# Optimization experiments

Hardware: AMD Instinct MI355X
Metric: run time of the kernel (lower is better)

The kernel has to match this reference:

```python
import jax, jax.numpy as jnp
import numpy as np

N = 50000   # nodes
E = 800000  # edges
D = 96      # feature dim


def setup_inputs() -> dict:
    key = jax.random.key(0)
    k1, k2, k3, k4 = jax.random.split(key, 4)
    scale = 1.0 / np.sqrt(D)
    return {
        "x": jax.random.normal(k1, (N, D), dtype=jnp.float32),
        "edge_index": jax.random.randint(k2, (2, E), 0, N, dtype=jnp.int64),
        "W1": jax.random.normal(k3, (D, D), dtype=jnp.float32) * scale,
        "b1": jnp.zeros((D,), dtype=jnp.float32),
        "W2": jax.random.normal(k4, (D, D), dtype=jnp.float32) * scale,
        "b2": jnp.zeros((D,), dtype=jnp.float32),
    }


def _gcn_conv(x, src, dst, W, b, n_nodes):
    # PyG GCNConv: linear transform, add self-loops, symmetric normalization,
    # scatter-add aggregation from src (row) to dst (col), then bias.
    h = x @ W  # [N, D_out]
    loops = jnp.arange(n_nodes, dtype=src.dtype)
    s = jnp.concatenate([src, loops])  # [E+N]
    d = jnp.concatenate([dst, loops])  # [E+N]
    deg = jax.ops.segment_sum(jnp.ones_like(d, dtype=h.dtype), d, num_segments=n_nodes)
    dinv = jnp.where(deg > 0, jax.lax.rsqrt(deg), 0.0)  # deg^-1/2, 0 for isolated
    norm = dinv[s] * dinv[d]  # [E+N]
    msg = norm[:, None] * h[s]  # gather + scale
    out = jax.ops.segment_sum(msg, d, num_segments=n_nodes)  # scatter-add
    return out + b


def reference(x, edge_index, W1, b1, W2, b2):
    src, dst = edge_index[0], edge_index[1]
    # dropout p=0.0 -> identity. ReLU after every layer (loop break never fires).
    h = _gcn_conv(x, src, dst, W1, b1, N)
    h = jax.nn.relu(h)
    h = _gcn_conv(h, src, dst, W2, b2, N)
    h = jax.nn.relu(h)
    return h
```

## Files before the change

### kernel.cpp

```cpp
#include <hip/hip_runtime.h>
#include <hip/hip_fp16.h>

#define NN 50000
#define EE 800000
#define DD 96

#define NBIN 196
#define CE   4096
#define CB   196
#define EPT2 16



__global__ __launch_bounds__(256) void k_hist(const int* __restrict__ ei,
                                              int* __restrict__ histB) {
    __shared__ int hist[NBIN];
    int t = threadIdx.x;
    if (t < NBIN) hist[t] = 0;
    __syncthreads();
    int e0 = blockIdx.x * CE;
#pragma unroll
    for (int k = 0; k < EPT2; ++k) {
        int e = e0 + k * 256 + t;
        if (e < EE) atomicAdd(&hist[ei[EE + e] >> 8], 1);
    }
    __syncthreads();
    if (t < NBIN) histB[t * CB + blockIdx.x] = hist[t];
}


__global__ __launch_bounds__(256) void k_scan_bins(int* __restrict__ histB,
                                                   int* __restrict__ binTot) {
    __shared__ int sh[256];
    int t = threadIdx.x;
    int b = blockIdx.x;
    int v = (t < CB) ? histB[b * CB + t] : 0;
    sh[t] = v;
    __syncthreads();
    for (int off = 1; off < 256; off <<= 1) {
        int u = (t >= off) ? sh[t - off] : 0;
        __syncthreads();
        sh[t] += u;
        __syncthreads();
    }
    if (t < CB) histB[b * CB + t] = sh[t] - v;
    if (t == 255) binTot[b] = sh[255];
}


__global__ __launch_bounds__(256) void k_scan_tot(const int* __restrict__ binTot,
                                                  int* __restrict__ binbase) {
    __shared__ int sh[256];
    int t = threadIdx.x;
    int v = (t < NBIN) ? binTot[t] : 0;
    sh[t] = v;
    __syncthreads();
    for (int off = 1; off < 256; off <<= 1) {
        int u = (t >= off) ? sh[t - off] : 0;
        __syncthreads();
        sh[t] += u;
        __syncthreads();
    }
    if (t < NBIN) binbase[t] = sh[t] - v;
    if (t == 0) binbase[NBIN] = EE;
}


__global__ __launch_bounds__(256) void k_scatter_bins(const int* __restrict__ ei,
                                                      const int* __restrict__ histB,
                                                      const int* __restrict__ binbase,
                                                      int* __restrict__ packed) {
    __shared__ int hist[NBIN];
    __shared__ int lofs[NBIN + 1];
    __shared__ int cur[NBIN];
    __shared__ int sstart[NBIN];
    __shared__ int buf[CE];
    __shared__ int sh[256];
    int t = threadIdx.x;
    int e0 = blockIdx.x * CE;
    int nE = min(CE, EE - e0);

    int s[EPT2], d[EPT2];
#pragma unroll
    for (int k = 0; k < EPT2; ++k) {
        int e = e0 + k * 256 + t;
        s[k] = (e < EE) ? ei[e] : 0;
        d[k] = (e < EE) ? ei[EE + e] : -1;
    }
    if (t < NBIN) hist[t] = 0;
    __syncthreads();
#pragma unroll
    for (int k = 0; k < EPT2; ++k)
        if (d[k] >= 0) atomicAdd(&hist[d[k] >> 8], 1);
    __syncthreads();
    int v = (t < NBIN) ? hist[t] : 0;
    sh[t] = v;
    __syncthreads();
    for (int off = 1; off < 256; off <<= 1) {
        int u = (t >= off) ? sh[t - off] : 0;
        __syncthreads();
        sh[t] += u;
        __syncthreads();
    }
    if (t < NBIN) { lofs[t] = sh[t] - v; cur[t] = sh[t] - v; }
    if (t == 0) lofs[NBIN] = nE;
    if (t < NBIN) sstart[t] = binbase[t] + histB[t * CB + blockIdx.x];
    __syncthreads();
#pragma unroll
    for (int k = 0; k < EPT2; ++k)
        if (d[k] >= 0) {
            int b = d[k] >> 8;
            int pos = atomicAdd(&cur[b], 1);
            buf[pos] = s[k] | ((d[k] & 0xFF) << 16);
        }
    __syncthreads();
    for (int i = t; i < nE; i += 256) {
        int blo = 0, bhi = NBIN;
        while (bhi - blo > 1) {
            int mid = (blo + bhi) >> 1;
            if (lofs[mid] <= i) blo = mid; else bhi = mid;
        }
        packed[sstart[blo] + (i - lofs[blo])] = buf[i];
    }
}


__global__ __launch_bounds__(256) void k_csr(const int* __restrict__ packed,
                                             const int* __restrict__ binbase,
                                             int* __restrict__ rp,
                                             float* __restrict__ dinv,
                                             int* __restrict__ col) {
    __shared__ int h256[256];
    __shared__ int excl[256];
    __shared__ int cur[256];
    __shared__ int sh[256];
    int t = threadIdx.x;
    int b = blockIdx.x;
    int base = binbase[b];
    int nE = binbase[b + 1] - base;

    h256[t] = 0;
    __syncthreads();
    for (int i = t; i < nE; i += 256)
        atomicAdd(&h256[(packed[base + i] >> 16) & 0xFF], 1);
    __syncthreads();
    int v = h256[t];
    sh[t] = v;
    __syncthreads();
    for (int off = 1; off < 256; off <<= 1) {
        int u = (t >= off) ? sh[t - off] : 0;
        __syncthreads();
        sh[t] += u;
        __syncthreads();
    }
    excl[t] = sh[t] - v;
    cur[t] = sh[t] - v;
    int node = b * 256 + t;
    if (node <= NN) rp[node] = base + excl[t];
    if (node < NN) dinv[node] = rsqrtf((float)(h256[t] + 1));
    __syncthreads();
    for (int i = t; i < nE; i += 256) {
        int pv = packed[base + i];
        int pos = atomicAdd(&cur[(pv >> 16) & 0xFF], 1);
        col[base + pos] = pv & 0xFFFF;
    }
}


__global__ void k_cvt(const float* __restrict__ x, const float* __restrict__ dinv,
                      __half* __restrict__ xh) {
    int i = blockIdx.x * blockDim.x + threadIdx.x;
    if (i < NN * 12) {
        int row = i / 12;
        float sc = dinv[row];
        const float4* xx = (const float4*)x;
        float4 f0 = xx[i * 2], f1 = xx[i * 2 + 1];
        __half h[8];
        h[0] = __float2half_rn(sc * f0.x); h[1] = __float2half_rn(sc * f0.y);
        h[2] = __float2half_rn(sc * f0.z); h[3] = __float2half_rn(sc * f0.w);
        h[4] = __float2half_rn(sc * f1.x); h[5] = __float2half_rn(sc * f1.y);
        h[6] = __float2half_rn(sc * f1.z); h[7] = __float2half_rn(sc * f1.w);
        ((uint4*)xh)[i] = *(uint4*)h;
    }
}


template <int FINAL>
__global__ __launch_bounds__(384) void k_fused(const __half* __restrict__ xh,
                                               const int* __restrict__ rp,
                                               const int* __restrict__ col,
                                               const float* __restrict__ dinv,
                                               const float* __restrict__ W,
                                               const float* __restrict__ b,
                                               __half* __restrict__ acth,
                                               float* __restrict__ outf) {
    __shared__ __half Wl[DD * DD];
    __shared__ float Al[32][100];
    int t = threadIdx.x;
    for (int i = t; i < DD * DD / 8; i += 384) {
        const float4* ww = (const float4*)W;
        float4 f0 = ww[i * 2], f1 = ww[i * 2 + 1];
        __half h[8];
        h[0] = __float2half_rn(f0.x); h[1] = __float2half_rn(f0.y);
        h[2] = __float2half_rn(f0.z); h[3] = __float2half_rn(f0.w);
        h[4] = __float2half_rn(f1.x); h[5] = __float2half_rn(f1.y);
        h[6] = __float2half_rn(f1.z); h[7] = __float2half_rn(f1.w);
        ((uint4*)Wl)[i] = *(uint4*)h;
    }

    int c  = t % 12;
    int ny = t / 12;
    int d = blockIdx.x * 32 + ny;
    const uint4* h4 = (const uint4*)xh;

    if (d < NN) {
        union U { uint4 u; __half2 h[4]; };
        float2 aA[4] = {{0,0},{0,0},{0,0},{0,0}};
        float2 aB[4] = {{0,0},{0,0},{0,0},{0,0}};
        int j0 = rp[d], j1 = rp[d + 1];
        int j = j0;
        for (; j + 3 < j1; j += 4) {
            int s0 = col[j], s1 = col[j+1], s2 = col[j+2], s3 = col[j+3];
            U v0, v1, v2, v3;
            v0.u = h4[s0 * 12 + c];
            v1.u = h4[s1 * 12 + c];
            v2.u = h4[s2 * 12 + c];
            v3.u = h4[s3 * 12 + c];
#pragma unroll
            for (int k = 0; k < 4; ++k) {
                float2 f0 = __half22float2(v0.h[k]);
                float2 f1 = __half22float2(v1.h[k]);
                float2 f2 = __half22float2(v2.h[k]);
                float2 f3 = __half22float2(v3.h[k]);
                aA[k].x += f0.x + f1.x; aA[k].y += f0.y + f1.y;
                aB[k].x += f2.x + f3.x; aB[k].y += f2.y + f3.y;
            }
        }
        for (; j < j1; ++j) {
            U v; v.u = h4[col[j] * 12 + c];
#pragma unroll
            for (int k = 0; k < 4; ++k) {
                float2 f = __half22float2(v.h[k]);
                aA[k].x += f.x; aA[k].y += f.y;
            }
        }
        U self; self.u = h4[d * 12 + c];
        float dd = dinv[d];
        float v[8];
#pragma unroll
        for (int k = 0; k < 4; ++k) {
            float2 fs = __half22float2(self.h[k]);
            v[2*k]   = dd * (aA[k].x + aB[k].x + fs.x);
            v[2*k+1] = dd * (aA[k].y + aB[k].y + fs.y);
        }
        *(float4*)&Al[ny][c * 8]     = make_float4(v[0], v[1], v[2], v[3]);
        *(float4*)&Al[ny][c * 8 + 4] = make_float4(v[4], v[5], v[6], v[7]);
    }
    __syncthreads();

    int tx = t % 24;
    int ry = t / 24;
    int c0 = tx * 4;
    float a0x = 0.f, a0y = 0.f, a0z = 0.f, a0w = 0.f;
    float a1x = 0.f, a1y = 0.f, a1z = 0.f, a1w = 0.f;
#pragma unroll 8
    for (int k = 0; k < DD; ++k) {
        uint2 wv = *(const uint2*)&Wl[k * DD + c0];
        const __half2* wh = (const __half2*)&wv;
        float2 w01 = __half22float2(wh[0]);
        float2 w23 = __half22float2(wh[1]);
        float r0 = Al[ry][k];
        float r1 = Al[ry + 16][k];
        a0x += r0 * w01.x; a0y += r0 * w01.y; a0z += r0 * w23.x; a0w += r0 * w23.y;
        a1x += r1 * w01.x; a1y += r1 * w01.y; a1z += r1 * w23.x; a1w += r1 * w23.y;
    }
    float4 bb = *(const float4*)&b[c0];
    int g0 = blockIdx.x * 32 + ry;
    int g1 = g0 + 16;
    float r0x = fmaxf(a0x + bb.x, 0.f), r0y = fmaxf(a0y + bb.y, 0.f);
    float r0z = fmaxf(a0z + bb.z, 0.f), r0w = fmaxf(a0w + bb.w, 0.f);
    float r1x = fmaxf(a1x + bb.x, 0.f), r1y = fmaxf(a1y + bb.y, 0.f);
    float r1z = fmaxf(a1z + bb.z, 0.f), r1w = fmaxf(a1w + bb.w, 0.f);
    if (g0 < NN) {
        if (FINAL) {
            *(float4*)&outf[g0 * DD + c0] = make_float4(r0x, r0y, r0z, r0w);
        } else {
            float sc = dinv[g0];
            __half h[4];
            h[0] = __float2half_rn(sc * r0x); h[1] = __float2half_rn(sc * r0y);
            h[2] = __float2half_rn(sc * r0z); h[3] = __float2half_rn(sc * r0w);
            *(uint2*)&acth[g0 * DD + c0] = *(uint2*)h;
        }
    }
    if (g1 < NN) {
        if (FINAL) {
            *(float4*)&outf[g1 * DD + c0] = make_float4(r1x, r1y, r1z, r1w);
        } else {
            float sc = dinv[g1];
            __half h[4];
            h[0] = __float2half_rn(sc * r1x); h[1] = __float2half_rn(sc * r1y);
            h[2] = __float2half_rn(sc * r1z); h[3] = __float2half_rn(sc * r1w);
            *(uint2*)&acth[g1 * DD + c0] = *(uint2*)h;
        }
    }
}


extern "C" void kernel_launch(void* const* d_in, const int* in_sizes, int n_in,
                              void* d_out, int out_size, void* d_ws, size_t ws_size,
                              hipStream_t stream) {
    const float* x  = (const float*)d_in[0];
    const int*   ei = (const int*)d_in[1];
    const float* W1 = (const float*)d_in[2];
    const float* b1 = (const float*)d_in[3];
    const float* W2 = (const float*)d_in[4];
    const float* b2 = (const float*)d_in[5];
    float* out = (float*)d_out;

    char* p = (char*)d_ws;
    int*   histB   = (int*)p;   p += ((size_t)NBIN * CB * 4 + 255) & ~(size_t)255;
    int*   binTot  = (int*)p;   p += ((size_t)NBIN * 4 + 255) & ~(size_t)255;
    int*   binbase = (int*)p;   p += ((size_t)(NBIN + 1) * 4 + 255) & ~(size_t)255;
    int*   rp      = (int*)p;   p += ((size_t)(NN + 1) * 4 + 255) & ~(size_t)255;
    float* dinv    = (float*)p; p += ((size_t)NN * 4 + 255) & ~(size_t)255;
    int*   col     = (int*)p;   p += ((size_t)EE * 4 + 255) & ~(size_t)255;
    __half* bufA   = (__half*)p; p += ((size_t)NN * DD * 2 + 255) & ~(size_t)255;
    __half* bufB   = (__half*)p;
    int*   packed  = (int*)bufA;

    k_hist<<<CB, 256, 0, stream>>>(ei, histB);
    k_scan_bins<<<NBIN, 256, 0, stream>>>(histB, binTot);
    k_scan_tot<<<1, 256, 0, stream>>>(binTot, binbase);
    k_scatter_bins<<<CB, 256, 0, stream>>>(ei, histB, binbase, packed);
    k_csr<<<NBIN, 256, 0, stream>>>(packed, binbase, rp, dinv, col);

    k_cvt<<<(NN * 12 + 255) / 256, 256, 0, stream>>>(x, dinv, bufA);

    k_fused<0><<<(NN + 31) / 32, 384, 0, stream>>>(bufA, rp, col, dinv, W1, b1,
                                                   bufB, nullptr);

    k_fused<1><<<(NN + 31) / 32, 384, 0, stream>>>(bufB, rp, col, dinv, W2, b2,
                                                   nullptr, out);
}
```

Measured before the change: 133.7 us.

## Fuse CSR-build and convert kernels into one cooperative kernel; unroll gather by 8

Six preprocessing kernels (histogram, two scans, bin scatter, CSR build, fp16 convert) become a single cooperative launch. The stages are separated by grid-wide syncs, and the first pass keeps each block's edges and local histogram in registers and shared memory. This removes several kernel launches and the reload of the edge list. In exchange it adds grid-sync overhead and requires all 196 blocks to be co-resident. Separately, the aggregation loop gathers 8 neighbours per iteration instead of 4 to raise memory-level parallelism, and launch_bounds now asks for 4 blocks per CU.

```diff
diff --git a/kernel.cpp b/kernel.cpp
--- a/kernel.cpp
+++ b/kernel.cpp
@@ -1,5 +1,8 @@
 #include <hip/hip_runtime.h>
 #include <hip/hip_fp16.h>
+#include <hip/hip_cooperative_groups.h>
+
+namespace cg = cooperative_groups;
 
 #define NN 50000
 #define EE 800000
@@ -12,64 +15,17 @@
 
 
 
-__global__ __launch_bounds__(256) void k_hist(const int* __restrict__ ei,
-                                              int* __restrict__ histB) {
-    __shared__ int hist[NBIN];
-    int t = threadIdx.x;
-    if (t < NBIN) hist[t] = 0;
-    __syncthreads();
-    int e0 = blockIdx.x * CE;
-#pragma unroll
-    for (int k = 0; k < EPT2; ++k) {
-        int e = e0 + k * 256 + t;
-        if (e < EE) atomicAdd(&hist[ei[EE + e] >> 8], 1);
-    }
-    __syncthreads();
-    if (t < NBIN) histB[t * CB + blockIdx.x] = hist[t];
-}
-
-
-__global__ __launch_bounds__(256) void k_scan_bins(int* __restrict__ histB,
-                                                   int* __restrict__ binTot) {
-    __shared__ int sh[256];
-    int t = threadIdx.x;
-    int b = blockIdx.x;
-    int v = (t < CB) ? histB[b * CB + t] : 0;
-    sh[t] = v;
-    __syncthreads();
-    for (int off = 1; off < 256; off <<= 1) {
-        int u = (t >= off) ? sh[t - off] : 0;
-        __syncthreads();
-        sh[t] += u;
-        __syncthreads();
-    }
-    if (t < CB) histB[b * CB + t] = sh[t] - v;
-    if (t == 255) binTot[b] = sh[255];
-}
-
-
-__global__ __launch_bounds__(256) void k_scan_tot(const int* __restrict__ binTot,
-                                                  int* __restrict__ binbase) {
-    __shared__ int sh[256];
-    int t = threadIdx.x;
-    int v = (t < NBIN) ? binTot[t] : 0;
-    sh[t] = v;
-    __syncthreads();
-    for (int off = 1; off < 256; off <<= 1) {
-        int u = (t >= off) ? sh[t - off] : 0;
-        __syncthreads();
-        sh[t] += u;
-        __syncthreads();
-    }
-    if (t < NBIN) binbase[t] = sh[t] - v;
-    if (t == 0) binbase[NBIN] = EE;
-}
-
-
-__global__ __launch_bounds__(256) void k_scatter_bins(const int* __restrict__ ei,
-                                                      const int* __restrict__ histB,
-                                                      const int* __restrict__ binbase,
-                                                      int* __restrict__ packed) {
+__global__ __launch_bounds__(256) void k_prep(const int* __restrict__ ei,
+                                              int* __restrict__ histB,
+                                              int* __restrict__ binTot,
+                                              int* __restrict__ binbase,
+                                              int* __restrict__ rp,
+                                              float* __restrict__ dinv,
+                                              int* __restrict__ col,
+                                              int* __restrict__ packed,
+                                              const float* __restrict__ x,
+                                              __half* __restrict__ xh) {
+    cg::grid_group grid = cg::this_grid();
     __shared__ int hist[NBIN];
     __shared__ int lofs[NBIN + 1];
     __shared__ int cur[NBIN];
@@ -77,100 +33,127 @@
     __shared__ int buf[CE];
     __shared__ int sh[256];
     int t = threadIdx.x;
-    int e0 = blockIdx.x * CE;
+    int blk = blockIdx.x;
+    int e0 = blk * CE;
     int nE = min(CE, EE - e0);
 
-    int s[EPT2], d[EPT2];
+    int s_[EPT2], d_[EPT2];
 #pragma unroll
     for (int k = 0; k < EPT2; ++k) {
         int e = e0 + k * 256 + t;
-        s[k] = (e < EE) ? ei[e] : 0;
-        d[k] = (e < EE) ? ei[EE + e] : -1;
-    }
+        s_[k] = (e < EE) ? ei[e] : 0;
+        d_[k] = (e < EE) ? ei[EE + e] : -1;
+    }
+
     if (t < NBIN) hist[t] = 0;
     __syncthreads();
 #pragma unroll
     for (int k = 0; k < EPT2; ++k)
-        if (d[k] >= 0) atomicAdd(&hist[d[k] >> 8], 1);
+        if (d_[k] >= 0) atomicAdd(&hist[d_[k] >> 8], 1);
     __syncthreads();
-    int v = (t < NBIN) ? hist[t] : 0;
-    sh[t] = v;
-    __syncthreads();
-    for (int off = 1; off < 256; off <<= 1) {
-        int u = (t >= off) ? sh[t - off] : 0;
-        __syncthreads();
-        sh[t] += u;
-        __syncthreads();
-    }
-    if (t < NBIN) { lofs[t] = sh[t] - v; cur[t] = sh[t] - v; }
-    if (t == 0) lofs[NBIN] = nE;
-    if (t < NBIN) sstart[t] = binbase[t] + histB[t * CB + blockIdx.x];
-    __syncthreads();
-#pragma unroll
-    for (int k = 0; k < EPT2; ++k)
-        if (d[k] >= 0) {
-            int b = d[k] >> 8;
-            int pos = atomicAdd(&cur[b], 1);
-            buf[pos] = s[k] | ((d[k] & 0xFF) << 16);
-        }
-    __syncthreads();
-    for (int i = t; i < nE; i += 256) {
-        int blo = 0, bhi = NBIN;
-        while (bhi - blo > 1) {
-            int mid = (blo + bhi) >> 1;
-            if (lofs[mid] <= i) blo = mid; else bhi = mid;
-        }
-        packed[sstart[blo] + (i - lofs[blo])] = buf[i];
-    }
-}
-
-
-__global__ __launch_bounds__(256) void k_csr(const int* __restrict__ packed,
-                                             const int* __restrict__ binbase,
-                                             int* __restrict__ rp,
-                                             float* __restrict__ dinv,
-                                             int* __restrict__ col) {
-    __shared__ int h256[256];
-    __shared__ int excl[256];
-    __shared__ int cur[256];
-    __shared__ int sh[256];
-    int t = threadIdx.x;
-    int b = blockIdx.x;
-    int base = binbase[b];
-    int nE = binbase[b + 1] - base;
-
-    h256[t] = 0;
-    __syncthreads();
-    for (int i = t; i < nE; i += 256)
-        atomicAdd(&h256[(packed[base + i] >> 16) & 0xFF], 1);
-    __syncthreads();
-    int v = h256[t];
-    sh[t] = v;
-    __syncthreads();
-    for (int off = 1; off < 256; off <<= 1) {
-        int u = (t >= off) ? sh[t - off] : 0;
-        __syncthreads();
-        sh[t] += u;
-        __syncthreads();
-    }
-    excl[t] = sh[t] - v;
-    cur[t] = sh[t] - v;
-    int node = b * 256 + t;
-    if (node <= NN) rp[node] = base + excl[t];
-    if (node < NN) dinv[node] = rsqrtf((float)(h256[t] + 1));
-    __syncthreads();
-    for (int i = t; i < nE; i += 256) {
-        int pv = packed[base + i];
-        int pos = atomicAdd(&cur[(pv >> 16) & 0xFF], 1);
-        col[base + pos] = pv & 0xFFFF;
-    }
-}
-
-
-__global__ void k_cvt(const float* __restrict__ x, const float* __restrict__ dinv,
-                      __half* __restrict__ xh) {
-    int i = blockIdx.x * blockDim.x + threadIdx.x;
-    if (i < NN * 12) {
+    if (t < NBIN) histB[t * CB + blk] = hist[t];
+    grid.sync();
+
+    {
+        int v = (t < CB) ? histB[blk * CB + t] : 0;
+        sh[t] = v;
+        __syncthreads();
+        for (int off = 1; off < 256; off <<= 1) {
+            int u = (t >= off) ? sh[t - off] : 0;
+            __syncthreads();
+            sh[t] += u;
+            __syncthreads();
+        }
+        if (t < CB) histB[blk * CB + t] = sh[t] - v;
+        if (t == 255) binTot[blk] = sh[255];
+    }
+    grid.sync();
+
+    if (blk == 0) {
+        int v = (t < NBIN) ? binTot[t] : 0;
+        sh[t] = v;
+        __syncthreads();
+        for (int off = 1; off < 256; off <<= 1) {
+            int u = (t >= off) ? sh[t - off] : 0;
+            __syncthreads();
+            sh[t] += u;
+            __syncthreads();
+        }
+        if (t < NBIN) binbase[t] = sh[t] - v;
+        if (t == 0) binbase[NBIN] = EE;
+    }
+    grid.sync();
+
+    {
+        int v = (t < NBIN) ? hist[t] : 0;
+        sh[t] = v;
+        __syncthreads();
+        for (int off = 1; off < 256; off <<= 1) {
+            int u = (t >= off) ? sh[t - off] : 0;
+            __syncthreads();
+            sh[t] += u;
+            __syncthreads();
+        }
+        if (t < NBIN) {
+            lofs[t] = sh[t] - v;
+            cur[t] = sh[t] - v;
+            sstart[t] = binbase[t] + histB[t * CB + blk];
+        }
+        if (t == 0) lofs[NBIN] = nE;
+        __syncthreads();
+#pragma unroll
+        for (int k = 0; k < EPT2; ++k)
+            if (d_[k] >= 0) {
+                int b = d_[k] >> 8;
+                int pos = atomicAdd(&cur[b], 1);
+                buf[pos] = s_[k] | ((d_[k] & 0xFF) << 16);
+            }
+        __syncthreads();
+        for (int i = t; i < nE; i += 256) {
+            int blo = 0, bhi = NBIN;
+            while (bhi - blo > 1) {
+                int mid = (blo + bhi) >> 1;
+                if (lofs[mid] <= i) blo = mid; else bhi = mid;
+            }
+            packed[sstart[blo] + (i - lofs[blo])] = buf[i];
+        }
+    }
+    grid.sync();
+
+    {
+        int base = binbase[blk];
+        int n = binbase[blk + 1] - base;
+        int* h256 = buf;
+        int* cur2 = buf + 256;
+        h256[t] = 0;
+        __syncthreads();
+        for (int i = t; i < n; i += 256)
+            atomicAdd(&h256[(packed[base + i] >> 16) & 0xFF], 1);
+        __syncthreads();
+        int v = h256[t];
+        sh[t] = v;
+        __syncthreads();
+        for (int off = 1; off < 256; off <<= 1) {
+            int u = (t >= off) ? sh[t - off] : 0;
+            __syncthreads();
+            sh[t] += u;
+            __syncthreads();
+        }
+        int ex = sh[t] - v;
+        cur2[t] = ex;
+        int node = blk * 256 + t;
+        if (node <= NN) rp[node] = base + ex;
+        if (node < NN) dinv[node] = rsqrtf((float)(v + 1));
+        __syncthreads();
+        for (int i = t; i < n; i += 256) {
+            int pv = packed[base + i];
+            int pos = atomicAdd(&cur2[(pv >> 16) & 0xFF], 1);
+            col[base + pos] = pv & 0xFFFF;
+        }
+    }
+    grid.sync();
+
+    for (int i = blk * 256 + t; i < NN * 12; i += CB * 256) {
         int row = i / 12;
         float sc = dinv[row];
         const float4* xx = (const float4*)x;
@@ -186,14 +169,14 @@
 
 
 template <int FINAL>
-__global__ __launch_bounds__(384) void k_fused(const __half* __restrict__ xh,
-                                               const int* __restrict__ rp,
-                                               const int* __restrict__ col,
-                                               const float* __restrict__ dinv,
-                                               const float* __restrict__ W,
-                                               const float* __restrict__ b,
-                                               __half* __restrict__ acth,
-                                               float* __restrict__ outf) {
+__global__ __launch_bounds__(384, 4) void k_fused(const __half* __restrict__ xh,
+                                                  const int* __restrict__ rp,
+                                                  const int* __restrict__ col,
+                                                  const float* __restrict__ dinv,
+                                                  const float* __restrict__ W,
+                                                  const float* __restrict__ b,
+                                                  __half* __restrict__ acth,
+                                                  float* __restrict__ outf) {
     __shared__ __half Wl[DD * DD];
     __shared__ float Al[32][100];
     int t = threadIdx.x;
@@ -219,6 +202,34 @@
         float2 aB[4] = {{0,0},{0,0},{0,0},{0,0}};
         int j0 = rp[d], j1 = rp[d + 1];
         int j = j0;
+        for (; j + 7 < j1; j += 8) {
+            int s0 = col[j],   s1 = col[j+1], s2 = col[j+2], s3 = col[j+3];
+            int s4 = col[j+4], s5 = col[j+5], s6 = col[j+6], s7 = col[j+7];
+            U v0, v1, v2, v3, v4, v5, v6, v7;
+            v0.u = h4[s0 * 12 + c];
+            v1.u = h4[s1 * 12 + c];
+            v2.u = h4[s2 * 12 + c];
+            v3.u = h4[s3 * 12 + c];
+            v4.u = h4[s4 * 12 + c];
+            v5.u = h4[s5 * 12 + c];
+            v6.u = h4[s6 * 12 + c];
+            v7.u = h4[s7 * 12 + c];
+#pragma unroll
+            for (int k = 0; k < 4; ++k) {
+                float2 f0 = __half22float2(v0.h[k]);
+                float2 f1 = __half22float2(v1.h[k]);
+                float2 f2 = __half22float2(v2.h[k]);
+                float2 f3 = __half22float2(v3.h[k]);
+                float2 f4 = __half22float2(v4.h[k]);
+                float2 f5 = __half22float2(v5.h[k]);
+                float2 f6 = __half22float2(v6.h[k]);
+                float2 f7 = __half22float2(v7.h[k]);
+                aA[k].x += (f0.x + f1.x) + (f4.x + f5.x);
+                aA[k].y += (f0.y + f1.y) + (f4.y + f5.y);
+                aB[k].x += (f2.x + f3.x) + (f6.x + f7.x);
+                aB[k].y += (f2.y + f3.y) + (f6.y + f7.y);
+            }
+        }
         for (; j + 3 < j1; j += 4) {
             int s0 = col[j], s1 = col[j+1], s2 = col[j+2], s3 = col[j+3];
             U v0, v1, v2, v3;
@@ -328,13 +339,11 @@
     __half* bufB   = (__half*)p;
     int*   packed  = (int*)bufA;
 
-    k_hist<<<CB, 256, 0, stream>>>(ei, histB);
-    k_scan_bins<<<NBIN, 256, 0, stream>>>(histB, binTot);
-    k_scan_tot<<<1, 256, 0, stream>>>(binTot, binbase);
-    k_scatter_bins<<<CB, 256, 0, stream>>>(ei, histB, binbase, packed);
-    k_csr<<<NBIN, 256, 0, stream>>>(packed, binbase, rp, dinv, col);
-
-    k_cvt<<<(NN * 12 + 255) / 256, 256, 0, stream>>>(x, dinv, bufA);
+    void* args[] = {(void*)&ei, (void*)&histB, (void*)&binTot, (void*)&binbase,
+                    (void*)&rp, (void*)&dinv, (void*)&col, (void*)&packed,
+                    (void*)&x, (void*)&bufA};
+    hipLaunchCooperativeKernel((const void*)k_prep, dim3(CB), dim3(256),
+                               args, 0, stream);
 
     k_fused<0><<<(NN + 31) / 32, 384, 0, stream>>>(bufA, rp, col, dinv, W1, b1,
                                                    bufB, nullptr);
```

Result: slower. 258.2 us (+93.2%).

## Fuse x-to-half conversion into CSR kernel and store aggregates as half in LDS

Applied to the files above, without the earlier changes.

The separate conversion kernel that scales x by deg^-1/2 and casts to half is folded into the CSR build kernel, which already holds each block's dinv values in shared memory. This removes one launch and the global re-read of dinv. The packed edge buffer moves to bufB so it does not clash with the half features now written in the same kernel. In the fused layer kernel the aggregated rows are kept in LDS as half instead of float, and the matmul loop reads two k values per iteration, which cuts LDS footprint and load count at the cost of extra rounding.

```diff
diff --git a/kernel.cpp b/kernel.cpp
--- a/kernel.cpp
+++ b/kernel.cpp
@@ -129,11 +129,13 @@
                                              const int* __restrict__ binbase,
                                              int* __restrict__ rp,
                                              float* __restrict__ dinv,
-                                             int* __restrict__ col) {
+                                             int* __restrict__ col,
+                                             const float* __restrict__ x,
+                                             __half* __restrict__ xh) {
     __shared__ int h256[256];
-    __shared__ int excl[256];
     __shared__ int cur[256];
     __shared__ int sh[256];
+    __shared__ float sdinv[256];
     int t = threadIdx.x;
     int b = blockIdx.x;
     int base = binbase[b];
@@ -153,34 +155,34 @@
         sh[t] += u;
         __syncthreads();
     }
-    excl[t] = sh[t] - v;
-    cur[t] = sh[t] - v;
+    int ex = sh[t] - v;
+    cur[t] = ex;
+    float di = rsqrtf((float)(v + 1));
+    sdinv[t] = di;
     int node = b * 256 + t;
-    if (node <= NN) rp[node] = base + excl[t];
-    if (node < NN) dinv[node] = rsqrtf((float)(h256[t] + 1));
+    if (node <= NN) rp[node] = base + ex;
+    if (node < NN) dinv[node] = di;
     __syncthreads();
     for (int i = t; i < nE; i += 256) {
         int pv = packed[base + i];
         int pos = atomicAdd(&cur[(pv >> 16) & 0xFF], 1);
         col[base + pos] = pv & 0xFFFF;
     }
-}
-
-
-__global__ void k_cvt(const float* __restrict__ x, const float* __restrict__ dinv,
-                      __half* __restrict__ xh) {
-    int i = blockIdx.x * blockDim.x + threadIdx.x;
-    if (i < NN * 12) {
-        int row = i / 12;
-        float sc = dinv[row];
-        const float4* xx = (const float4*)x;
-        float4 f0 = xx[i * 2], f1 = xx[i * 2 + 1];
-        __half h[8];
-        h[0] = __float2half_rn(sc * f0.x); h[1] = __float2half_rn(sc * f0.y);
-        h[2] = __float2half_rn(sc * f0.z); h[3] = __float2half_rn(sc * f0.w);
-        h[4] = __float2half_rn(sc * f1.x); h[5] = __float2half_rn(sc * f1.y);
-        h[6] = __float2half_rn(sc * f1.z); h[7] = __float2half_rn(sc * f1.w);
-        ((uint4*)xh)[i] = *(uint4*)h;
+    for (int i = t; i < 256 * 12; i += 256) {
+        int rr = i / 12;
+        int cc = i % 12;
+        int r = b * 256 + rr;
+        if (r < NN) {
+            float sc = sdinv[rr];
+            const float4* xx = (const float4*)x + (size_t)r * 24 + cc * 2;
+            float4 f0 = xx[0], f1 = xx[1];
+            __half h[8];
+            h[0] = __float2half_rn(sc * f0.x); h[1] = __float2half_rn(sc * f0.y);
+            h[2] = __float2half_rn(sc * f0.z); h[3] = __float2half_rn(sc * f0.w);
+            h[4] = __float2half_rn(sc * f1.x); h[5] = __float2half_rn(sc * f1.y);
+            h[6] = __float2half_rn(sc * f1.z); h[7] = __float2half_rn(sc * f1.w);
+            ((uint4*)xh)[(size_t)r * 12 + cc] = *(uint4*)h;
+        }
     }
 }
 
@@ -195,7 +197,7 @@
                                                __half* __restrict__ acth,
                                                float* __restrict__ outf) {
     __shared__ __half Wl[DD * DD];
-    __shared__ float Al[32][100];
+    __shared__ __half Al[32][104];
     int t = threadIdx.x;
     for (int i = t; i < DD * DD / 8; i += 384) {
         const float4* ww = (const float4*)W;
@@ -246,15 +248,14 @@
         }
         U self; self.u = h4[d * 12 + c];
         float dd = dinv[d];
-        float v[8];
+        __half hv[8];
 #pragma unroll
         for (int k = 0; k < 4; ++k) {
             float2 fs = __half22float2(self.h[k]);
-            v[2*k]   = dd * (aA[k].x + aB[k].x + fs.x);
-            v[2*k+1] = dd * (aA[k].y + aB[k].y + fs.y);
-        }
-        *(float4*)&Al[ny][c * 8]     = make_float4(v[0], v[1], v[2], v[3]);
-        *(float4*)&Al[ny][c * 8 + 4] = make_float4(v[4], v[5], v[6], v[7]);
+            hv[2*k]   = __float2half_rn(dd * (aA[k].x + aB[k].x + fs.x));
+            hv[2*k+1] = __float2half_rn(dd * (aA[k].y + aB[k].y + fs.y));
+        }
+        *(uint4*)&Al[ny][c * 8] = *(uint4*)hv;
     }
     __syncthreads();
 
@@ -263,16 +264,26 @@
     int c0 = tx * 4;
     float a0x = 0.f, a0y = 0.f, a0z = 0.f, a0w = 0.f;
     float a1x = 0.f, a1y = 0.f, a1z = 0.f, a1w = 0.f;
-#pragma unroll 8
-    for (int k = 0; k < DD; ++k) {
-        uint2 wv = *(const uint2*)&Wl[k * DD + c0];
-        const __half2* wh = (const __half2*)&wv;
-        float2 w01 = __half22float2(wh[0]);
-        float2 w23 = __half22float2(wh[1]);
-        float r0 = Al[ry][k];
-        float r1 = Al[ry + 16][k];
-        a0x += r0 * w01.x; a0y += r0 * w01.y; a0z += r0 * w23.x; a0w += r0 * w23.y;
-        a1x += r1 * w01.x; a1y += r1 * w01.y; a1z += r1 * w23.x; a1w += r1 * w23.y;
+#pragma unroll 4
+    for (int k = 0; k < DD; k += 2) {
+        uint2 wv0 = *(const uint2*)&Wl[k * DD + c0];
+        uint2 wv1 = *(const uint2*)&Wl[(k + 1) * DD + c0];
+        const __half2* wh0 = (const __half2*)&wv0;
+        const __half2* wh1 = (const __half2*)&wv1;
+        float2 w0a = __half22float2(wh0[0]);
+        float2 w0b = __half22float2(wh0[1]);
+        float2 w1a = __half22float2(wh1[0]);
+        float2 w1b = __half22float2(wh1[1]);
+        float2 ra = __half22float2(*(const __half2*)&Al[ry][k]);
+        float2 rb = __half22float2(*(const __half2*)&Al[ry + 16][k]);
+        a0x += ra.x * w0a.x + ra.y * w1a.x;
+        a0y += ra.x * w0a.y + ra.y * w1a.y;
+        a0z += ra.x * w0b.x + ra.y * w1b.x;
+        a0w += ra.x * w0b.y + ra.y * w1b.y;
+        a1x += rb.x * w0a.x + rb.y * w1a.x;
+        a1y += rb.x * w0a.y + rb.y * w1a.y;
+        a1z += rb.x * w0b.x + rb.y * w1b.x;
+        a1w += rb.x * w0b.y + rb.y * w1b.y;
     }
     float4 bb = *(const float4*)&b[c0];
     int g0 = blockIdx.x * 32 + ry;
@@ -326,15 +337,13 @@
     int*   col     = (int*)p;   p += ((size_t)EE * 4 + 255) & ~(size_t)255;
     __half* bufA   = (__half*)p; p += ((size_t)NN * DD * 2 + 255) & ~(size_t)255;
     __half* bufB   = (__half*)p;
-    int*   packed  = (int*)bufA;
+    int*   packed  = (int*)bufB;
 
     k_hist<<<CB, 256, 0, stream>>>(ei, histB);
     k_scan_bins<<<NBIN, 256, 0, stream>>>(histB, binTot);
     k_scan_tot<<<1, 256, 0, stream>>>(binTot, binbase);
     k_scatter_bins<<<CB, 256, 0, stream>>>(ei, histB, binbase, packed);
-    k_csr<<<NBIN, 256, 0, stream>>>(packed, binbase, rp, dinv, col);
-
-    k_cvt<<<(NN * 12 + 255) / 256, 256, 0, stream>>>(x, dinv, bufA);
+    k_csr<<<NBIN, 256, 0, stream>>>(packed, binbase, rp, dinv, col, x, bufA);
 
     k_fused<0><<<(NN + 31) / 32, 384, 0, stream>>>(bufA, rp, col, dinv, W1, b1,
                                                    bufB, nullptr);
```

Result: slower. 147.2 us (+10.2%).
